# Kernel tuning notes

Hardware: AMD Instinct MI355X
Metric: run time of the kernel (lower is better)

## Reference

```python
import jax, jax.numpy as jnp
import numpy as np

DIM = 2048
N_HEADS = 16
KV_HEADS = 2 * 2  # 4
HEAD_DIM = DIM // N_HEADS  # 128
B, T = 2, 2048


def apply_rope(x, cos, sin):
    # Faithful to the source: x is replaced by its rotated version, then
    # multiplied by (sin + cos). x: [B,H,T,D], cos/sin: [T,D] broadcast.
    x1 = x[..., ::2]
    x2 = x[..., 1::2]
    rot = jnp.stack((-x2, x1), axis=-1).reshape(x.shape)
    return rot * sin + rot * cos


def setup_inputs() -> dict:
    key = jax.random.key(0)
    ks = jax.random.split(key, 8)
    x = jax.random.normal(ks[0], (B, T, DIM), dtype=jnp.float32)
    cos = jax.random.uniform(ks[1], (T, HEAD_DIM), dtype=jnp.float32)
    sin = jax.random.uniform(ks[2], (T, HEAD_DIM), dtype=jnp.float32)
    mask = jnp.tril(jnp.ones((T, T), dtype=bool))  # causal
    s = 1.0 / np.sqrt(DIM)
    Wq = jax.random.normal(ks[3], (DIM, DIM), dtype=jnp.float32) * s
    Wk = jax.random.normal(ks[4], (KV_HEADS * HEAD_DIM, DIM), dtype=jnp.float32) * s
    Wv = jax.random.normal(ks[5], (KV_HEADS * HEAD_DIM, DIM), dtype=jnp.float32) * s
    Wout = jax.random.normal(ks[6], (DIM, DIM), dtype=jnp.float32) * s
    bout = jax.random.normal(ks[7], (DIM,), dtype=jnp.float32) * s
    return {"x": x, "cos": cos, "sin": sin, "mask": mask,
            "Wq": Wq, "Wk": Wk, "Wv": Wv, "Wout": Wout, "bout": bout}


def reference(x, cos, sin, mask, Wq, Wk, Wv, Wout, bout):
    Bb, Tt, C = x.shape
    # projections (torch Linear: x @ W.T)
    q = (x @ Wq.T).reshape(Bb, Tt, N_HEADS, HEAD_DIM).transpose(0, 2, 1, 3)
    k = (x @ Wk.T).reshape(Bb, Tt, KV_HEADS, HEAD_DIM).transpose(0, 2, 1, 3)
    v = (x @ Wv.T).reshape(Bb, Tt, KV_HEADS, HEAD_DIM).transpose(0, 2, 1, 3)
    q = apply_rope(q, cos, sin)
    k = apply_rope(k, cos, sin)
    repeat = N_HEADS // KV_HEADS
    k = jnp.repeat(k, repeat, axis=1)  # [B,H,T,D]
    v = jnp.repeat(v, repeat, axis=1)
    attn = jnp.einsum("bhtd,bhsd->bhts", q, k) / np.sqrt(HEAD_DIM)
    attn = jnp.where(mask, attn, jnp.float32(-1e9))
    probs = jax.nn.softmax(attn, axis=-1)
    out = jnp.einsum("bhts,bhsd->bhtd", probs, v)
    out = out.transpose(0, 2, 1, 3).reshape(Bb, Tt, C)
    return out @ Wout.T + bout
```

## Files before the change

kernel.cpp:

```cpp
#include <hip/hip_runtime.h>
#include <type_traits>

#define DEVI __device__ __forceinline__

typedef unsigned short u16;
typedef unsigned int u32;
typedef float f32x4 __attribute__((ext_vector_type(4)));
typedef __bf16 bf16x8 __attribute__((ext_vector_type(8)));
typedef unsigned short u16x4 __attribute__((ext_vector_type(4)));
typedef unsigned short u16x8 __attribute__((ext_vector_type(8)));
typedef unsigned int u32x2 __attribute__((ext_vector_type(2)));

constexpr int BATCH = 2;
constexpr int T     = 2048;
constexpr int DIM   = 2048;
constexpr int NH    = 16;
constexpr int KVH   = 4;
constexpr int HD    = 128;
constexpr int NQKV  = DIM + 2 * KVH * HD;
constexpr int ROWS  = BATCH * T;
constexpr float SC2 = 0.08838834764831845f * 1.4426950408889634f;

DEVI u16 f2b(float f) {
  u32 u = __float_as_uint(f);
  return (u16)((u + 0x7fffu + ((u >> 16) & 1u)) >> 16);
}
DEVI float b2f(u16 u) { return __uint_as_float(((u32)u) << 16); }

DEVI u32 cvtpk(float lo, float hi) {
  u32 r;
  asm("v_cvt_pk_bf16_f32 %0, %1, %2" : "=v"(r) : "v"(lo), "v"(hi));
  return r;
}

DEVI f32x4 mfma16(bf16x8 a, bf16x8 b, f32x4 c) {
  return __builtin_amdgcn_mfma_f32_16x16x32_bf16(a, b, c, 0, 0, 0);
}
DEVI void gload16(const void* g, void* l) {
  __builtin_amdgcn_global_load_lds((const __attribute__((address_space(1))) void*)g,
                                   (__attribute__((address_space(3))) void*)l, 16, 0, 0);
}

__global__ void cvt_all_kernel(const float* __restrict__ x,
                               const float* __restrict__ Wq, const float* __restrict__ Wk,
                               const float* __restrict__ Wv, const float* __restrict__ Wo,
                               const float* __restrict__ cosp, const float* __restrict__ sinp,
                               u16* __restrict__ xb, u16* __restrict__ wqkv,
                               u16* __restrict__ wout, float* __restrict__ cs)
{
  constexpr int S0 = ROWS * DIM / 4;
  constexpr int S1 = DIM * DIM / 4;
  constexpr int S2 = 512 * DIM / 4;
  constexpr int S3 = 512 * DIM / 4;
  constexpr int S4 = DIM * DIM / 4;
  constexpr int S5 = T * HD / 4;
  int i = blockIdx.x * 256 + threadIdx.x;
  const float* src; u16* dst;
  if (i < S0) { src = x; dst = xb; }
  else if ((i -= S0) < S1) { src = Wq; dst = wqkv; }
  else if ((i -= S1) < S2) { src = Wk; dst = wqkv + DIM * DIM; }
  else if ((i -= S2) < S3) { src = Wv; dst = wqkv + (size_t)(DIM + 512) * DIM; }
  else if ((i -= S3) < S4) { src = Wo; dst = wout; }
  else if ((i -= S4) < S5) {
    float4 c = ((const float4*)cosp)[i];
    float4 s = ((const float4*)sinp)[i];
    float4 o = { c.x + s.x, c.y + s.y, c.z + s.z, c.w + s.w };
    ((float4*)cs)[i] = o;
    return;
  } else return;
  float4 v = ((const float4*)src)[i];
  u16x4 o = { f2b(v.x), f2b(v.y), f2b(v.z), f2b(v.w) };
  ((u16x4*)dst)[i] = o;
}

template<bool BF16OUT, bool BIAS>
__global__ __launch_bounds__(256) void gemm_bt_kernel(
    const u16* __restrict__ A, const u16* __restrict__ W,
    void* __restrict__ Cout, const float* __restrict__ bias,
    int M, int N, int K)
{
  constexpr int BK = 64;
  __shared__ u16 sA[128 * BK];
  __shared__ u16 sB[128 * BK];
  const int nbx = N >> 7;
  const int bx = blockIdx.x % nbx;
  const int by = blockIdx.x / nbx;
  const int m0 = by << 7, n0 = bx << 7;
  const int tid = threadIdx.x;
  const int w = tid >> 6, lane = tid & 63;
  const int wr = w >> 1, wc = w & 1;
  const int lq = lane & 15, lg = lane >> 4;

  f32x4 acc[4][4] = {};

  int srow[4], scb[4];
#pragma unroll
  for (int c = 0; c < 4; ++c) {
    int off = (w * 4 + c) * 1024 + lane * 16;
    srow[c] = off >> 7;
    scb[c]  = (off & 127) ^ ((srow[c] & 7) << 4);
  }

  for (int kt = 0; kt < K; kt += BK) {
#pragma unroll
    for (int c = 0; c < 4; ++c) {
      u16* la = sA + (w * 4 + c) * 512;
      u16* lb = sB + (w * 4 + c) * 512;
      gload16(A + (size_t)(m0 + srow[c]) * K + kt + (scb[c] >> 1), la);
      gload16(W + (size_t)(n0 + srow[c]) * K + kt + (scb[c] >> 1), lb);
    }
    __syncthreads();
#pragma unroll
    for (int ks = 0; ks < 2; ++ks) {
      bf16x8 af[4], bfr[4];
#pragma unroll
      for (int i = 0; i < 4; ++i) {
        int ra = wr * 64 + i * 16 + lq;
        int ca = (ks * 64 + lg * 16) ^ ((ra & 7) << 4);
        af[i] = *(const bf16x8*)((const char*)sA + ra * 128 + ca);
        int rb = wc * 64 + i * 16 + lq;
        int cb = (ks * 64 + lg * 16) ^ ((rb & 7) << 4);
        bfr[i] = *(const bf16x8*)((const char*)sB + rb * 128 + cb);
      }
#pragma unroll
      for (int i = 0; i < 4; ++i)
#pragma unroll
        for (int j = 0; j < 4; ++j)
          acc[i][j] = mfma16(af[i], bfr[j], acc[i][j]);
    }
    __syncthreads();
  }

  const int crow = m0 + wr * 64 + lg * 4;
  const int ccol = n0 + wc * 64 + lq;
#pragma unroll
  for (int j = 0; j < 4; ++j) {
    int col = ccol + j * 16;
    float bv = BIAS ? bias[col] : 0.0f;
#pragma unroll
    for (int i = 0; i < 4; ++i)
#pragma unroll
      for (int r = 0; r < 4; ++r) {
        size_t idx = (size_t)(crow + i * 16 + r) * N + col;
        float v = acc[i][j][r] + bv;
        if (BF16OUT) ((u16*)Cout)[idx] = f2b(v);
        else         ((float*)Cout)[idx] = v;
      }
  }
}

__global__ void rope_k_kernel(const u16* __restrict__ Y, const float* __restrict__ cs,
                              u16* __restrict__ kr)
{
  int pid = blockIdx.x * 256 + threadIdx.x;
  int i  = pid & 63;
  int hr = pid >> 6;
  int h  = hr & (KVH - 1);
  int r  = hr / KVH;
  int t  = r & (T - 1);
  int b  = r >> 11;
  u32 y = *(const u32*)(Y + (size_t)r * NQKV + DIM + h * HD + 2 * i);
  float y0 = b2f((u16)(y & 0xffffu));
  float y1 = b2f((u16)(y >> 16));
  const float* cp = cs + t * HD + 2 * i;
  u32 o = (u32)f2b(-y1 * cp[0]) | ((u32)f2b(y0 * cp[1]) << 16);
  *(u32*)(kr + (((size_t)(b * KVH + h) * T + t) * HD + 2 * i)) = o;
}

__global__ __launch_bounds__(256) void vt_kernel(const u16* __restrict__ Y, u16* __restrict__ vt)
{
  __shared__ u16 tile[64][136];
  const int tid = threadIdx.x;
  const int tc = blockIdx.x & 31;
  const int kh = (blockIdx.x >> 5) & 3;
  const int b  = blockIdx.x >> 7;
  const u16* src = Y + (size_t)(b * T + tc * 64) * NQKV + (DIM + KVH * HD) + kh * HD;
#pragma unroll
  for (int pass = 0; pass < 4; ++pass) {
    int r = pass * 16 + (tid >> 4);
    int c = (tid & 15) * 8;
    *(u16x8*)&tile[r][c] = *(const u16x8*)(src + (size_t)r * NQKV + c);
  }
  __syncthreads();
  const int d = tid >> 1, th = tid & 1;
  u16* dst = vt + ((size_t)((b * KVH + kh) * HD + d) * T) + tc * 64 + th * 32;
#pragma unroll
  for (int j = 0; j < 4; ++j) {
    u16x8 v;
#pragma unroll
    for (int e = 0; e < 8; ++e) v[e] = tile[th * 32 + j * 8 + e][d];
    *(u16x8*)(dst + j * 8) = v;
  }
}

__global__ __launch_bounds__(256, 2) void attn_kernel(
    const u16* __restrict__ Y, const float* __restrict__ cs,
    const u16* __restrict__ Kr, const u16* __restrict__ Vt,
    u16* __restrict__ Aout)
{
  __shared__ u16 ldsK[2][64 * 128];
  __shared__ u16 ldsV[2][128 * 64];
  __shared__ u16 ldsP[4][32 * 40];

  const int tid = threadIdx.x;
  const int w = tid >> 6, lane = tid & 63;
  const int lq = lane & 15, lg = lane >> 4;

  const int s  = blockIdx.x & 255;
  const int r0 = blockIdx.x >> 8;
  const int x  = s & 7;
  const int j  = s >> 3;
  const int bh = (x >> 2) * 16 + (x & 3) * 4 + (j & 3);
  const int p  = r0 ? (8 + (j >> 2)) : (j >> 2);
  const int b = bh >> 4, h = bh & 15, kh = h >> 2;
  const int qcA = p, qcB = 31 - p;
  const int rowA = qcA * 64 + w * 16;
  const int rowB = qcB * 64 + w * 16;
  const int nst = qcB + 1;

  bf16x8 qf[2][4];
#pragma unroll
  for (int qg = 0; qg < 2; ++qg) {
    const int rowX = qg ? rowB : rowA;
    const u16* yp = Y + ((size_t)(b * T + rowX + lq)) * NQKV + h * HD + lg * 8;
    const float* cp = cs + (rowX + lq) * HD + lg * 8;
#pragma unroll
    for (int ds = 0; ds < 4; ++ds) {
      u16x8 y = *(const u16x8*)(yp + ds * 32);
      float4 c0 = *(const float4*)(cp + ds * 32);
      float4 c1 = *(const float4*)(cp + ds * 32 + 4);
      u16x8 o;
      o[0] = f2b(-b2f(y[1]) * c0.x * SC2); o[1] = f2b(b2f(y[0]) * c0.y * SC2);
      o[2] = f2b(-b2f(y[3]) * c0.z * SC2); o[3] = f2b(b2f(y[2]) * c0.w * SC2);
      o[4] = f2b(-b2f(y[5]) * c1.x * SC2); o[5] = f2b(b2f(y[4]) * c1.y * SC2);
      o[6] = f2b(-b2f(y[7]) * c1.z * SC2); o[7] = f2b(b2f(y[6]) * c1.w * SC2);
      qf[qg][ds] = *(bf16x8*)&o;
    }
  }

  const u16* Kg = Kr + (size_t)(b * KVH + kh) * T * HD;
  const u16* Vg = Vt + (size_t)(b * KVH + kh) * HD * T;

  int kgo[4], klb[4], vgo[4], vlb[4];
  {
    const int vr = lane >> 3, vc = lane & 7;
#pragma unroll
    for (int i = 0; i < 4; ++i) {
      int krow = w * 16 + i * 4 + lg;
      kgo[i] = krow * HD + (((lq * 16) ^ ((krow & 7) << 4)) >> 1);
      klb[i] = (w * 16 + i * 4) * 128;
      int vrow = w * 32 + i * 8 + vr;
      vgo[i] = vrow * T + (((vc * 16) ^ ((vr & 7) << 4)) >> 1);
      vlb[i] = (w * 32 + i * 8) * 64;
    }
  }

  f32x4 accO[2][8] = {};
  float lsum[2] = { 0.f, 0.f };

#pragma unroll
  for (int i = 0; i < 4; ++i) {
    gload16(Kg + kgo[i], &ldsK[0][klb[i]]);
    gload16(Vg + vgo[i], &ldsV[0][vlb[i]]);
  }
  __syncthreads();

  int cur = 0;
  for (int t = 0; t < nst; ++t) {
    if (t + 1 < nst) {
      const u16* Kt  = Kg + (size_t)(t + 1) * 64 * HD;
      const u16* Vts = Vg + (t + 1) * 64;
#pragma unroll
      for (int i = 0; i < 4; ++i) {
        gload16(Kt + kgo[i],  &ldsK[cur ^ 1][klb[i]]);
        gload16(Vts + vgo[i], &ldsV[cur ^ 1][vlb[i]]);
      }
    }
    const int s0 = t << 6;
    const u16* Kb = ldsK[cur];
    const u16* Vb = ldsV[cur];

    auto softmax_qg = [&](f32x4 (&s4)[4], int qidx, bool diag, float& ls,
                          float (&pp)[16]) {
      if (diag) {
#pragma unroll
        for (int si = 0; si < 4; ++si)
#pragma unroll
          for (int r = 0; r < 4; ++r) {
            int sidx = s0 + si * 16 + lg * 4 + r;
            pp[si * 4 + r] = (sidx <= qidx) ? __builtin_amdgcn_exp2f(s4[si][r]) : 0.0f;
          }
      } else {
#pragma unroll
        for (int si = 0; si < 4; ++si)
#pragma unroll
          for (int r = 0; r < 4; ++r)
            pp[si * 4 + r] = __builtin_amdgcn_exp2f(s4[si][r]);
      }
      float ps = 0.f;
#pragma unroll
      for (int i2 = 0; i2 < 16; ++i2) ps += pp[i2];
      ls += ps;
    };

    auto tile_body = [&](auto hasA_c) {
      constexpr bool HASA = decltype(hasA_c)::value;
      f32x4 aS[2][4] = {};
#pragma unroll
      for (int si = 0; si < 4; ++si)
#pragma unroll
        for (int ds = 0; ds < 4; ++ds) {
          const u16* kp = Kb + (si * 16 + lq) * 128 +
                          (((ds * 64 + lg * 16) ^ ((lq & 7) << 4)) >> 1);
          bf16x8 kf = *(const bf16x8*)kp;
          if constexpr (HASA) aS[0][si] = mfma16(kf, qf[0][ds], aS[0][si]);
          aS[1][si] = mfma16(kf, qf[1][ds], aS[1][si]);
        }

      float pp[2][16];
      if constexpr (HASA)
        softmax_qg(aS[0], rowA + lq, t == qcA, lsum[0], pp[0]);
      softmax_qg(aS[1], rowB + lq, t == qcB, lsum[1], pp[1]);

#pragma unroll
      for (int ks = 0; ks < 2; ++ks) {
        if constexpr (HASA) {
          u16* pw = &ldsP[w][lq * 40];
          u32x2 wa = { cvtpk(pp[0][8 * ks + 0], pp[0][8 * ks + 1]),
                       cvtpk(pp[0][8 * ks + 2], pp[0][8 * ks + 3]) };
          u32x2 wb = { cvtpk(pp[0][8 * ks + 4], pp[0][8 * ks + 5]),
                       cvtpk(pp[0][8 * ks + 6], pp[0][8 * ks + 7]) };
          *(u32x2*)(pw + lg * 4)      = wa;
          *(u32x2*)(pw + 16 + lg * 4) = wb;
        }
        {
          u16* pw = &ldsP[w][(16 + lq) * 40];
          u32x2 wa = { cvtpk(pp[1][8 * ks + 0], pp[1][8 * ks + 1]),
                       cvtpk(pp[1][8 * ks + 2], pp[1][8 * ks + 3]) };
          u32x2 wb = { cvtpk(pp[1][8 * ks + 4], pp[1][8 * ks + 5]),
                       cvtpk(pp[1][8 * ks + 6], pp[1][8 * ks + 7]) };
          *(u32x2*)(pw + lg * 4)      = wa;
          *(u32x2*)(pw + 16 + lg * 4) = wb;
        }
        asm volatile("" ::: "memory");
        bf16x8 pf0, pf1;
        if constexpr (HASA) pf0 = *(const bf16x8*)(&ldsP[w][lq * 40] + lg * 8);
        pf1 = *(const bf16x8*)(&ldsP[w][(16 + lq) * 40] + lg * 8);
        asm volatile("" ::: "memory");
#pragma unroll
        for (int db = 0; db < 8; ++db) {
          const u16* vp = Vb + (db * 16 + lq) * 64 +
                          (((ks * 64 + lg * 16) ^ ((lq & 7) << 4)) >> 1);
          bf16x8 vf = *(const bf16x8*)vp;
          if constexpr (HASA) accO[0][db] = mfma16(vf, pf0, accO[0][db]);
          accO[1][db] = mfma16(vf, pf1, accO[1][db]);
        }
      }
    };

    if (t <= qcA) tile_body(std::integral_constant<bool, true>{});
    else          tile_body(std::integral_constant<bool, false>{});

    __syncthreads();
    cur ^= 1;
  }

#pragma unroll
  for (int qg = 0; qg < 2; ++qg) {
    const int rowX = qg ? rowB : rowA;
    float l = qg ? lsum[1] : lsum[0];
    l += __shfl_xor(l, 16);
    l += __shfl_xor(l, 32);
    float inv = 1.0f / l;
    u16* Ab = Aout + ((size_t)b * T + rowX + lq) * DIM + h * HD;
#pragma unroll
    for (int db = 0; db < 8; ++db) {
      f32x4 a = qg ? accO[1][db] : accO[0][db];
      u32x2 st = { cvtpk(a[0] * inv, a[1] * inv),
                   cvtpk(a[2] * inv, a[3] * inv) };
      *(u32x2*)(Ab + db * 16 + lg * 4) = st;
    }
  }
}

extern "C" void kernel_launch(void* const* d_in, const int* in_sizes, int n_in,
                              void* d_out, int out_size, void* d_ws, size_t ws_size,
                              hipStream_t stream) {
  const float* x    = (const float*)d_in[0];
  const float* cosp = (const float*)d_in[1];
  const float* sinp = (const float*)d_in[2];
  const float* Wq   = (const float*)d_in[4];
  const float* Wk   = (const float*)d_in[5];
  const float* Wv   = (const float*)d_in[6];
  const float* Wo   = (const float*)d_in[7];
  const float* bo   = (const float*)d_in[8];

  char* ws = (char*)d_ws;
  u16*   xb   = (u16*)(ws + 0);
  u16*   wqkv = (u16*)(ws + 16777216);
  u16*   wout = (u16*)(ws + 29360128);
  float* cs   = (float*)(ws + 37748736);
  u16*   yqkv = (u16*)(ws + 38797312);
  u16*   kr   = (u16*)(ws + 63963136);
  u16*   vt   = (u16*)(ws + 68157440);
  u16* aout = xb;

  constexpr int CVT_TOTAL = ROWS * DIM / 4 + DIM * DIM / 4 + 512 * DIM / 4 * 2
                          + DIM * DIM / 4 + T * HD / 4;
  cvt_all_kernel<<<(CVT_TOTAL + 255) / 256, 256, 0, stream>>>(
      x, Wq, Wk, Wv, Wo, cosp, sinp, xb, wqkv, wout, cs);

  gemm_bt_kernel<true, false><<<(ROWS / 128) * (NQKV / 128), 256, 0, stream>>>(
      xb, wqkv, yqkv, nullptr, ROWS, NQKV, DIM);

  rope_k_kernel<<<ROWS * KVH * 64 / 256, 256, 0, stream>>>(yqkv, cs, kr);
  vt_kernel<<<BATCH * KVH * (T / 64), 256, 0, stream>>>(yqkv, vt);

  attn_kernel<<<BATCH * NH * 16, 256, 0, stream>>>(yqkv, cs, kr, vt, aout);

  gemm_bt_kernel<false, true><<<(ROWS / 128) * (DIM / 128), 256, 0, stream>>>(
      aout, wout, d_out, bo, ROWS, DIM, DIM);
}
```

Measured before the change: 192.6 us.

## Use 512-thread attention blocks covering 128-row query chunks to share K/V tiles

The attention kernel now runs 8 waves per block, with each block handling two 128-row query chunks (paired for causal balance) instead of two 64-row chunks. Each K/V tile loaded into LDS is reused by twice as many query rows, which halves the global-to-LDS traffic per query. Each wave issues half as many loads. Per-wave diagonal indices handle the causal mask, and waves whose rows are fully masked skip compute while still joining the barriers. The cost is half as many blocks, at one block per CU, and some waves sitting idle on the last tiles, which may reduce latency hiding.

```diff
diff --git a/kernel.cpp b/kernel.cpp
--- a/kernel.cpp
+++ b/kernel.cpp
@@ -193,30 +193,29 @@
   }
 }
 
-__global__ __launch_bounds__(256, 2) void attn_kernel(
+__global__ __launch_bounds__(512, 1) void attn_kernel(
     const u16* __restrict__ Y, const float* __restrict__ cs,
     const u16* __restrict__ Kr, const u16* __restrict__ Vt,
     u16* __restrict__ Aout)
 {
   __shared__ u16 ldsK[2][64 * 128];
   __shared__ u16 ldsV[2][128 * 64];
-  __shared__ u16 ldsP[4][32 * 40];
+  __shared__ u16 ldsP[8][32 * 40];
 
   const int tid = threadIdx.x;
   const int w = tid >> 6, lane = tid & 63;
   const int lq = lane & 15, lg = lane >> 4;
 
-  const int s  = blockIdx.x & 255;
-  const int r0 = blockIdx.x >> 8;
-  const int x  = s & 7;
-  const int j  = s >> 3;
+  const int x  = blockIdx.x & 7;
+  const int j  = blockIdx.x >> 3;
   const int bh = (x >> 2) * 16 + (x & 3) * 4 + (j & 3);
-  const int p  = r0 ? (8 + (j >> 2)) : (j >> 2);
+  const int p  = j >> 2;
   const int b = bh >> 4, h = bh & 15, kh = h >> 2;
-  const int qcA = p, qcB = 31 - p;
-  const int rowA = qcA * 64 + w * 16;
-  const int rowB = qcB * 64 + w * 16;
-  const int nst = qcB + 1;
+  const int rowA = p * 128 + w * 16;
+  const int rowB = (15 - p) * 128 + w * 16;
+  const int diagA = rowA >> 6;
+  const int diagB = rowB >> 6;
+  const int nst = (16 - p) * 2;
 
   bf16x8 qf[2][4];
 #pragma unroll
@@ -241,17 +240,19 @@
   const u16* Kg = Kr + (size_t)(b * KVH + kh) * T * HD;
   const u16* Vg = Vt + (size_t)(b * KVH + kh) * HD * T;
 
-  int kgo[4], klb[4], vgo[4], vlb[4];
+  int kgo[2], klb[2], vgo[2], vlb[2];
   {
-    const int vr = lane >> 3, vc = lane & 7;
-#pragma unroll
-    for (int i = 0; i < 4; ++i) {
-      int krow = w * 16 + i * 4 + lg;
+    const int kr4 = lane >> 4;
+    const int vr8 = lane >> 3;
+    const int vc = lane & 7;
+#pragma unroll
+    for (int i = 0; i < 2; ++i) {
+      int krow = w * 8 + i * 4 + kr4;
       kgo[i] = krow * HD + (((lq * 16) ^ ((krow & 7) << 4)) >> 1);
-      klb[i] = (w * 16 + i * 4) * 128;
-      int vrow = w * 32 + i * 8 + vr;
-      vgo[i] = vrow * T + (((vc * 16) ^ ((vr & 7) << 4)) >> 1);
-      vlb[i] = (w * 32 + i * 8) * 64;
+      klb[i] = (w * 8 + i * 4) * 128;
+      int vrow = w * 16 + i * 8 + vr8;
+      vgo[i] = vrow * T + (((vc * 16) ^ ((vrow & 7) << 4)) >> 1);
+      vlb[i] = (w * 16 + i * 8) * 64;
     }
   }
 
@@ -259,7 +260,7 @@
   float lsum[2] = { 0.f, 0.f };
 
 #pragma unroll
-  for (int i = 0; i < 4; ++i) {
+  for (int i = 0; i < 2; ++i) {
     gload16(Kg + kgo[i], &ldsK[0][klb[i]]);
     gload16(Vg + vgo[i], &ldsV[0][vlb[i]]);
   }
@@ -271,7 +272,7 @@
       const u16* Kt  = Kg + (size_t)(t + 1) * 64 * HD;
       const u16* Vts = Vg + (t + 1) * 64;
 #pragma unroll
-      for (int i = 0; i < 4; ++i) {
+      for (int i = 0; i < 2; ++i) {
         gload16(Kt + kgo[i],  &ldsK[cur ^ 1][klb[i]]);
         gload16(Vts + vgo[i], &ldsV[cur ^ 1][vlb[i]]);
       }
@@ -319,8 +320,8 @@
 
       float pp[2][16];
       if constexpr (HASA)
-        softmax_qg(aS[0], rowA + lq, t == qcA, lsum[0], pp[0]);
-      softmax_qg(aS[1], rowB + lq, t == qcB, lsum[1], pp[1]);
+        softmax_qg(aS[0], rowA + lq, t == diagA, lsum[0], pp[0]);
+      softmax_qg(aS[1], rowB + lq, t == diagB, lsum[1], pp[1]);
 
 #pragma unroll
       for (int ks = 0; ks < 2; ++ks) {
@@ -358,8 +359,8 @@
       }
     };
 
-    if (t <= qcA) tile_body(std::integral_constant<bool, true>{});
-    else          tile_body(std::integral_constant<bool, false>{});
+    if (t <= diagA)      tile_body(std::integral_constant<bool, true>{});
+    else if (t <= diagB) tile_body(std::integral_constant<bool, false>{});
 
     __syncthreads();
     cur ^= 1;
@@ -416,7 +417,7 @@
   rope_k_kernel<<<ROWS * KVH * 64 / 256, 256, 0, stream>>>(yqkv, cs, kr);
   vt_kernel<<<BATCH * KVH * (T / 64), 256, 0, stream>>>(yqkv, vt);
 
-  attn_kernel<<<BATCH * NH * 16, 256, 0, stream>>>(yqkv, cs, kr, vt, aout);
+  attn_kernel<<<BATCH * NH * 8, 512, 0, stream>>>(yqkv, cs, kr, vt, aout);
 
   gemm_bt_kernel<false, true><<<(ROWS / 128) * (DIM / 128), 256, 0, stream>>>(
       aout, wout, d_out, bo, ROWS, DIM, DIM);
```

Result: no change. 194.8 us (+1.2%).

## Replace K/V double buffering with single-buffer split-phase loads in attention

Applied to the files above, without the earlier changes.

Halves the LDS footprint for K and V by using single buffers instead of double buffers. V for the current tile is loaded at the start of each iteration and overlaps the QK^T phase. The next K tile is loaded after an added barrier and overlaps the PV phase. The intent is to cut LDS use so more blocks can be resident per CU, at the cost of an extra barrier per iteration and less latency hiding for V.

```diff
diff --git a/kernel.cpp b/kernel.cpp
--- a/kernel.cpp
+++ b/kernel.cpp
@@ -198,8 +198,8 @@
     const u16* __restrict__ Kr, const u16* __restrict__ Vt,
     u16* __restrict__ Aout)
 {
-  __shared__ u16 ldsK[2][64 * 128];
-  __shared__ u16 ldsV[2][128 * 64];
+  __shared__ u16 ldsK[64 * 128];
+  __shared__ u16 ldsV[128 * 64];
   __shared__ u16 ldsP[4][32 * 40];
 
   const int tid = threadIdx.x;
@@ -259,26 +259,17 @@
   float lsum[2] = { 0.f, 0.f };
 
 #pragma unroll
-  for (int i = 0; i < 4; ++i) {
-    gload16(Kg + kgo[i], &ldsK[0][klb[i]]);
-    gload16(Vg + vgo[i], &ldsV[0][vlb[i]]);
-  }
+  for (int i = 0; i < 4; ++i) gload16(Kg + kgo[i], &ldsK[klb[i]]);
   __syncthreads();
 
-  int cur = 0;
   for (int t = 0; t < nst; ++t) {
-    if (t + 1 < nst) {
-      const u16* Kt  = Kg + (size_t)(t + 1) * 64 * HD;
-      const u16* Vts = Vg + (t + 1) * 64;
-#pragma unroll
-      for (int i = 0; i < 4; ++i) {
-        gload16(Kt + kgo[i],  &ldsK[cur ^ 1][klb[i]]);
-        gload16(Vts + vgo[i], &ldsV[cur ^ 1][vlb[i]]);
-      }
-    }
     const int s0 = t << 6;
-    const u16* Kb = ldsK[cur];
-    const u16* Vb = ldsV[cur];
+
+    {
+      const u16* Vts = Vg + t * 64;
+#pragma unroll
+      for (int i = 0; i < 4; ++i) gload16(Vts + vgo[i], &ldsV[vlb[i]]);
+    }
 
     auto softmax_qg = [&](f32x4 (&s4)[4], int qidx, bool diag, float& ls,
                           float (&pp)[16]) {
@@ -303,25 +294,39 @@
       ls += ps;
     };
 
-    auto tile_body = [&](auto hasA_c) {
+    float pp[2][16];
+    const bool hasA = (t <= qcA);
+
+    auto qk_phase = [&](auto hasA_c) {
       constexpr bool HASA = decltype(hasA_c)::value;
       f32x4 aS[2][4] = {};
 #pragma unroll
       for (int si = 0; si < 4; ++si)
 #pragma unroll
         for (int ds = 0; ds < 4; ++ds) {
-          const u16* kp = Kb + (si * 16 + lq) * 128 +
+          const u16* kp = ldsK + (si * 16 + lq) * 128 +
                           (((ds * 64 + lg * 16) ^ ((lq & 7) << 4)) >> 1);
           bf16x8 kf = *(const bf16x8*)kp;
           if constexpr (HASA) aS[0][si] = mfma16(kf, qf[0][ds], aS[0][si]);
           aS[1][si] = mfma16(kf, qf[1][ds], aS[1][si]);
         }
-
-      float pp[2][16];
       if constexpr (HASA)
         softmax_qg(aS[0], rowA + lq, t == qcA, lsum[0], pp[0]);
       softmax_qg(aS[1], rowB + lq, t == qcB, lsum[1], pp[1]);
-
+    };
+    if (hasA) qk_phase(std::integral_constant<bool, true>{});
+    else      qk_phase(std::integral_constant<bool, false>{});
+
+    __syncthreads();
+
+    if (t + 1 < nst) {
+      const u16* Kt = Kg + (size_t)(t + 1) * 64 * HD;
+#pragma unroll
+      for (int i = 0; i < 4; ++i) gload16(Kt + kgo[i], &ldsK[klb[i]]);
+    }
+
+    auto pv_phase = [&](auto hasA_c) {
+      constexpr bool HASA = decltype(hasA_c)::value;
 #pragma unroll
       for (int ks = 0; ks < 2; ++ks) {
         if constexpr (HASA) {
@@ -349,7 +354,7 @@
         asm volatile("" ::: "memory");
 #pragma unroll
         for (int db = 0; db < 8; ++db) {
-          const u16* vp = Vb + (db * 16 + lq) * 64 +
+          const u16* vp = ldsV + (db * 16 + lq) * 64 +
                           (((ks * 64 + lg * 16) ^ ((lq & 7) << 4)) >> 1);
           bf16x8 vf = *(const bf16x8*)vp;
           if constexpr (HASA) accO[0][db] = mfma16(vf, pf0, accO[0][db]);
@@ -357,12 +362,10 @@
         }
       }
     };
-
-    if (t <= qcA) tile_body(std::integral_constant<bool, true>{});
-    else          tile_body(std::integral_constant<bool, false>{});
+    if (hasA) pv_phase(std::integral_constant<bool, true>{});
+    else      pv_phase(std::integral_constant<bool, false>{});
 
     __syncthreads();
-    cur ^= 1;
   }
 
 #pragma unroll
```

Result: no change. 192.2 us (-0.2%).
